# Kernel optimization log

Hardware: AMD Instinct MI355X
Metric: run time of the kernel (lower is better)

## Reference

```python
import jax, jax.numpy as jnp
import numpy as np

KB, KI = 6, 0   # kernel quantizer: quantized_bits(6, 0, alpha=1)
BB, BI = 6, 0   # bias quantizer:   quantized_bits(6, 0, alpha=1)
AB, AI = 6, 0   # activation:       quantized_relu(6, 0)


def _round_ste(p):
    # straight-through round (QKeras _round_through); tf.round and jnp.round
    # both round half-to-even
    return p + jax.lax.stop_gradient(jnp.round(p) - p)


def quantized_bits(x, bits, integer):
    # QKeras quantized_bits with keep_negative=1, symmetric=0, alpha=1
    m = float(2 ** (bits - 1))      # non-sign levels
    m_i = float(2 ** integer)
    p = x * (m / m_i)
    return (m_i / m) * jnp.clip(_round_ste(p), -m, m - 1.0)


def quantized_relu(x, bits, integer):
    # QKeras quantized_relu with negative_slope=0, use_sigmoid=0
    m = float(2 ** bits)
    m_i = float(2 ** integer)
    p = x * (m / m_i)
    return (m_i / m) * jnp.clip(_round_ste(p), 0.0, m - 1.0)


def setup_inputs() -> dict:
    key = jax.random.key(0)
    ks = jax.random.split(key, 9)
    dims = [128, 1024, 2048, 4096, 4096]
    inp = {"x": jax.random.normal(ks[0], (8192, dims[0]), dtype=jnp.float32)}
    for i in range(4):
        fan_in, fan_out = dims[i], dims[i + 1]
        scale = np.sqrt(2.0 / (fan_in + fan_out))  # glorot-ish scale
        inp[f"W{i}"] = jax.random.normal(ks[1 + 2 * i], (fan_in, fan_out), dtype=jnp.float32) * scale
        inp[f"b{i}"] = jax.random.normal(ks[2 + 2 * i], (fan_out,), dtype=jnp.float32) * 0.01
    return inp


def reference(x, W0, b0, W1, b1, W2, b2, W3, b3):
    Ws = [W0, W1, W2, W3]
    bs = [b0, b1, b2, b3]
    h = x
    for i in range(4):
        wq = quantized_bits(Ws[i], KB, KI)
        bq = quantized_bits(bs[i], BB, BI)
        h = jnp.dot(h, wq) + bq
        if i != 3:  # last layer has activation=None
            h = quantized_relu(h, AB, AI)
    return h
```

## Files before the change

kernel.cpp:

```cpp
#include <hip/hip_runtime.h>
#include <stdint.h>

typedef int v4i __attribute__((ext_vector_type(4)));

__device__ __forceinline__ float qlevel(float x) {
  float p = rintf(x * 32.0f);
  return fminf(fmaxf(p, -32.0f), 31.0f);
}

__device__ __forceinline__ int8_t qrelu_level(float p) {
  int q = (int)rintf(p);
  q = q < 0 ? 0 : (q > 63 ? 63 : q);
  return (int8_t)q;
}

__device__ __forceinline__ void async16(const void* g, void* l) {
  __builtin_amdgcn_global_load_lds(
      (const __attribute__((address_space(1))) void*)g,
      (__attribute__((address_space(3))) void*)l, 16, 0, 0);
}

__global__ __launch_bounds__(256) void quant_w0_k(const float* __restrict__ W,
                                                  int8_t* __restrict__ wq) {
  int i = blockIdx.x * 256 + threadIdx.x;
  float4 v = ((const float4*)W)[i];
  char4 c;
  c.x = (int8_t)(int)qlevel(v.x);
  c.y = (int8_t)(int)qlevel(v.y);
  c.z = (int8_t)(int)qlevel(v.z);
  c.w = (int8_t)(int)qlevel(v.w);
  ((char4*)wq)[i] = c;
}

__global__ __launch_bounds__(256) void quantT_k(const float* __restrict__ W,
                                                int8_t* __restrict__ wt,
                                                int K, int N) {
  const int t = threadIdx.x;
  const int l = t & 63;
  const int kc = t >> 6;
  const int k0 = blockIdx.y * 64 + kc * 16;
  const int n = blockIdx.x * 64 + l;
  union { int8_t b[16]; int4 v; } u;
#pragma unroll
  for (int j = 0; j < 16; ++j)
    u.b[j] = (int8_t)(int)qlevel(W[(size_t)(k0 + j) * N + n]);
  *(int4*)&wt[(size_t)n * K + k0] = u.v;
}

__global__ __launch_bounds__(256) void quant_bias_k(
    const float* __restrict__ b0, const float* __restrict__ b1,
    const float* __restrict__ b2, const float* __restrict__ b3,
    float* __restrict__ o0, float* __restrict__ o1,
    float* __restrict__ o2, float* __restrict__ o3) {
  int i = blockIdx.x * 256 + threadIdx.x;
  if (i < 1024) o0[i] = qlevel(b0[i]);
  if (i < 2048) o1[i] = qlevel(b1[i]);
  o2[i] = qlevel(b2[i]);
  o3[i] = qlevel(b3[i]);
}

__global__ __launch_bounds__(256) void layer0_k(const float* __restrict__ x,
                                                const int8_t* __restrict__ w0q,
                                                const float* __restrict__ bint,
                                                int8_t* __restrict__ a1) {
  const int K = 128, N = 1024;
  __shared__ float xs[64][132];
  __shared__ int8_t wsm[128][64];
  const int tid = threadIdx.x;
  const int m0 = blockIdx.y * 64;
  const int n0 = blockIdx.x * 64;
#pragma unroll
  for (int i = 0; i < 8; ++i) {
    int idx = tid + 256 * i;
    int row = idx >> 5, c4 = idx & 31;
    float4 v = *(const float4*)(x + (size_t)(m0 + row) * K + c4 * 4);
    *(float4*)&xs[row][c4 * 4] = v;
  }
#pragma unroll
  for (int i = 0; i < 8; ++i) {
    int idx = tid + 256 * i;
    int k = idx >> 4, c4 = idx & 15;
    *(int*)&wsm[k][c4 * 4] = *(const int*)(w0q + (size_t)k * N + n0 + c4 * 4);
  }
  __syncthreads();
  const int ty = tid >> 4, tx = tid & 15;
  float acc[4][4] = {};
  for (int k4 = 0; k4 < K; k4 += 4) {
    float xr[4][4];
#pragma unroll
    for (int i = 0; i < 4; ++i) {
      float4 v = *(const float4*)&xs[ty * 4 + i][k4];
      xr[i][0] = v.x; xr[i][1] = v.y; xr[i][2] = v.z; xr[i][3] = v.w;
    }
#pragma unroll
    for (int kk = 0; kk < 4; ++kk) {
      char4 cv = *(const char4*)&wsm[k4 + kk][tx * 4];
      float w0 = (float)cv.x, w1 = (float)cv.y, w2 = (float)cv.z, w3 = (float)cv.w;
#pragma unroll
      for (int i = 0; i < 4; ++i) {
        acc[i][0] = fmaf(xr[i][kk], w0, acc[i][0]);
        acc[i][1] = fmaf(xr[i][kk], w1, acc[i][1]);
        acc[i][2] = fmaf(xr[i][kk], w2, acc[i][2]);
        acc[i][3] = fmaf(xr[i][kk], w3, acc[i][3]);
      }
    }
  }
  const int n = n0 + tx * 4;
  float b0v = 2.0f * bint[n + 0], b1v = 2.0f * bint[n + 1];
  float b2v = 2.0f * bint[n + 2], b3v = 2.0f * bint[n + 3];
#pragma unroll
  for (int i = 0; i < 4; ++i) {
    int m = m0 + ty * 4 + i;
    char4 o;
    o.x = qrelu_level(2.0f * acc[i][0] + b0v);
    o.y = qrelu_level(2.0f * acc[i][1] + b1v);
    o.z = qrelu_level(2.0f * acc[i][2] + b2v);
    o.w = qrelu_level(2.0f * acc[i][3] + b3v);
    *(char4*)&a1[(size_t)m * 1024 + n] = o;
  }
}

template <bool FINAL>
__global__ __launch_bounds__(512) void gemm_i8(const int8_t* __restrict__ A,
                                               const int8_t* __restrict__ BT,
                                               const float* __restrict__ bint,
                                               void* __restrict__ outp,
                                               int M, int N, int K) {
  __shared__ __align__(16) int8_t ldsA[3][256 * 64];
  __shared__ __align__(16) int8_t ldsB[3][256 * 64];
  const int tid = threadIdx.x;
  const int wid = tid >> 6;
  const int lane = tid & 63;
  const int wm = wid >> 2, wn = wid & 3;
  const int quad = lane >> 4, r = lane & 15;
  const int m0 = blockIdx.y * 256, n0 = blockIdx.x * 256;

  const int8_t* Ab = A + (size_t)m0 * K;
  const int8_t* Bb = BT + (size_t)n0 * K;

  const int srow = tid >> 2;
  const int sp = tid & 3;
  const int skc = (sp - (srow >> 1)) & 3;
  const int8_t* gA0 = Ab + (size_t)srow * K + skc * 16;
  const int8_t* gA1 = Ab + (size_t)(srow + 128) * K + skc * 16;
  const int8_t* gB0 = Bb + (size_t)srow * K + skc * 16;
  const int8_t* gB1 = Bb + (size_t)(srow + 128) * K + skc * 16;
  const int ldsOff0 = (wid * 64) * 16;
  const int ldsOff1 = (512 + wid * 64) * 16;

  const int pfrag = (quad + (r >> 1)) & 3;

  v4i acc[8][4] = {};

#define STAGE(buf, kt)                                \
  do {                                                \
    async16(gA0 + (kt) * 64, &ldsA[buf][ldsOff0]);    \
    async16(gA1 + (kt) * 64, &ldsA[buf][ldsOff1]);    \
    async16(gB0 + (kt) * 64, &ldsB[buf][ldsOff0]);    \
    async16(gB1 + (kt) * 64, &ldsB[buf][ldsOff1]);    \
  } while (0)

#define ITER(p, q, kt, doStage, vmN)                                          \
  do {                                                                        \
    __builtin_amdgcn_s_barrier();                                             \
    v4i bf[4], af0[4], af1[4];                                                \
    const int8_t* La_ = &ldsA[p][0];                                          \
    const int8_t* Lb_ = &ldsB[p][0];                                          \
    _Pragma("unroll")                                                         \
    for (int nt = 0; nt < 4; ++nt)                                            \
      bf[nt] = *(const v4i*)&Lb_[(wn * 64 + nt * 16 + r) * 64 + pfrag * 16];  \
    _Pragma("unroll")                                                         \
    for (int mt = 0; mt < 4; ++mt)                                            \
      af0[mt] = *(const v4i*)&La_[(wm * 128 + mt * 16 + r) * 64 + pfrag * 16];\
    _Pragma("unroll")                                                         \
    for (int mt = 0; mt < 4; ++mt)                                            \
      af1[mt] = *(const v4i*)&La_[(wm * 128 + 64 + mt * 16 + r) * 64 +        \
                                  pfrag * 16];                                \
    if (doStage) STAGE(q, kt);                                                \
    __builtin_amdgcn_s_setprio(1);                                            \
    _Pragma("unroll")                                                         \
    for (int mt = 0; mt < 4; ++mt)                                            \
      _Pragma("unroll")                                                       \
      for (int nt = 0; nt < 4; ++nt)                                          \
        acc[mt][nt] = __builtin_amdgcn_mfma_i32_16x16x64_i8(                  \
            af0[mt], bf[nt], acc[mt][nt], 0, 0, 0);                           \
    _Pragma("unroll")                                                         \
    for (int mt = 0; mt < 4; ++mt)                                            \
      _Pragma("unroll")                                                       \
      for (int nt = 0; nt < 4; ++nt)                                          \
        acc[4 + mt][nt] = __builtin_amdgcn_mfma_i32_16x16x64_i8(              \
            af1[mt], bf[nt], acc[4 + mt][nt], 0, 0, 0);                       \
    __builtin_amdgcn_s_setprio(0);                                            \
    if (vmN == 4) asm volatile("s_waitcnt vmcnt(4)" ::: "memory");            \
    if (vmN == 0) asm volatile("s_waitcnt vmcnt(0)" ::: "memory");            \
  } while (0)

  const int NT = K >> 6;

  STAGE(0, 0);
  STAGE(1, 1);
  asm volatile("s_waitcnt vmcnt(4)" ::: "memory");

  for (int t = 0; t < NT - 2; ++t) {
    ITER(t % 3, (t + 2) % 3, t + 2, true, 4);
  }
  ITER((NT - 2) % 3, 0, 0, false, 0);
  ITER((NT - 1) % 3, 0, 0, false, -1);

#undef ITER
#undef STAGE

  const int mbase = m0 + wm * 128;
  const int nbase = n0 + wn * 64;
  if (FINAL) {
    float* out = (float*)outp;
#pragma unroll
    for (int nt = 0; nt < 4; ++nt) {
      int n = nbase + nt * 16 + r;
      float bq = bint[n] * 0.03125f;
#pragma unroll
      for (int mt = 0; mt < 8; ++mt)
#pragma unroll
        for (int g = 0; g < 4; ++g) {
          int m = mbase + mt * 16 + quad * 4 + g;
          out[(size_t)m * N + n] = (float)acc[mt][nt][g] * (1.0f / 2048.0f) + bq;
        }
    }
  } else {
    int8_t* out = (int8_t*)outp;
#pragma unroll
    for (int nt = 0; nt < 4; ++nt) {
      int n = nbase + nt * 16 + r;
      float b2 = 2.0f * bint[n];
#pragma unroll
      for (int mt = 0; mt < 8; ++mt)
#pragma unroll
        for (int g = 0; g < 4; ++g) {
          int m = mbase + mt * 16 + quad * 4 + g;
          out[(size_t)m * N + n] =
              qrelu_level((float)acc[mt][nt][g] * 0.03125f + b2);
        }
    }
  }
}

extern "C" void kernel_launch(void* const* d_in, const int* in_sizes, int n_in,
                              void* d_out, int out_size, void* d_ws, size_t ws_size,
                              hipStream_t stream) {
  const float* x  = (const float*)d_in[0];
  const float* W0 = (const float*)d_in[1];
  const float* b0 = (const float*)d_in[2];
  const float* W1 = (const float*)d_in[3];
  const float* b1 = (const float*)d_in[4];
  const float* W2 = (const float*)d_in[5];
  const float* b2 = (const float*)d_in[6];
  const float* W3 = (const float*)d_in[7];
  const float* b3 = (const float*)d_in[8];

  uint8_t* ws = (uint8_t*)d_ws;
  int8_t* wq0 = (int8_t*)(ws + 0);
  int8_t* wt1 = (int8_t*)(ws + 131072);
  int8_t* wt2 = (int8_t*)(ws + 2228224);
  int8_t* wt3 = (int8_t*)(ws + 10616832);
  float*  bq0 = (float*)(ws + 27394048);
  float*  bq1 = (float*)(ws + 27398144);
  float*  bq2 = (float*)(ws + 27406336);
  float*  bq3 = (float*)(ws + 27422720);
  int8_t* a1  = (int8_t*)(ws + 27439104);
  int8_t* a2  = (int8_t*)(ws + 35827712);
  int8_t* a3  = (int8_t*)(ws + 52604928);

  quant_w0_k<<<128, 256, 0, stream>>>(W0, wq0);
  quantT_k<<<dim3(2048 / 64, 1024 / 64), 256, 0, stream>>>(W1, wt1, 1024, 2048);
  quantT_k<<<dim3(4096 / 64, 2048 / 64), 256, 0, stream>>>(W2, wt2, 2048, 4096);
  quantT_k<<<dim3(4096 / 64, 4096 / 64), 256, 0, stream>>>(W3, wt3, 4096, 4096);
  quant_bias_k<<<16, 256, 0, stream>>>(b0, b1, b2, b3, bq0, bq1, bq2, bq3);
  layer0_k<<<dim3(16, 128), 256, 0, stream>>>(x, wq0, bq0, a1);
  gemm_i8<false><<<dim3(2048 / 256, 8192 / 256), 512, 0, stream>>>(
      a1, wt1, bq1, a2, 8192, 2048, 1024);
  gemm_i8<false><<<dim3(4096 / 256, 8192 / 256), 512, 0, stream>>>(
      a2, wt2, bq2, a3, 8192, 4096, 2048);
  gemm_i8<true><<<dim3(4096 / 256, 8192 / 256), 512, 0, stream>>>(
      a3, wt3, bq3, d_out, 8192, 4096, 4096);
}
```

Measured before the change: 459.8 us.

## Software-pipeline LDS fragment reads with MFMA via register double-buffering

The int8 GEMM main loop now keeps the A and B fragments for the current k-tile in a register array. The LDS reads for the next k-tile are interleaved between the MFMA groups, so LDS latency overlaps with matrix math instead of running as a separate read phase before the MFMAs. The global-to-LDS staging is issued at the top of each iteration. Each iteration now ends with a full vmcnt(0) wait and a barrier, which shortens how far the global prefetch can run ahead and adds register pressure from the live fragment array.

```diff
diff --git a/kernel.cpp b/kernel.cpp
--- a/kernel.cpp
+++ b/kernel.cpp
@@ -151,6 +151,7 @@
   const int pfrag = (quad + (r >> 1)) & 3;
 
   v4i acc[8][4] = {};
+  v4i fr[12];
 
 #define STAGE(buf, kt)                                \
   do {                                                \
@@ -160,54 +161,70 @@
     async16(gB1 + (kt) * 64, &ldsB[buf][ldsOff1]);    \
   } while (0)
 
-#define ITER(p, q, kt, doStage, vmN)                                          \
+#define RDA0(Lx, mt) (*(const v4i*)&(Lx)[(wm * 128 + (mt) * 16 + r) * 64 + pfrag * 16])
+#define RDA1(Lx, mt) (*(const v4i*)&(Lx)[(wm * 128 + 64 + (mt) * 16 + r) * 64 + pfrag * 16])
+#define RDB(Lx, nt)  (*(const v4i*)&(Lx)[(wn * 64 + (nt) * 16 + r) * 64 + pfrag * 16])
+
+#define MG(ai, ar)                                                            \
+  _Pragma("unroll")                                                           \
+  for (int nt = 0; nt < 4; ++nt)                                              \
+    acc[ar][nt] = __builtin_amdgcn_mfma_i32_16x16x64_i8(fr[ai], fr[nt],       \
+                                                        acc[ar][nt], 0, 0, 0);
+
+#define BODY(REF, LnA, LnB)                                                   \
   do {                                                                        \
-    __builtin_amdgcn_s_barrier();                                             \
-    v4i bf[4], af0[4], af1[4];                                                \
-    const int8_t* La_ = &ldsA[p][0];                                          \
-    const int8_t* Lb_ = &ldsB[p][0];                                          \
-    _Pragma("unroll")                                                         \
-    for (int nt = 0; nt < 4; ++nt)                                            \
-      bf[nt] = *(const v4i*)&Lb_[(wn * 64 + nt * 16 + r) * 64 + pfrag * 16];  \
-    _Pragma("unroll")                                                         \
-    for (int mt = 0; mt < 4; ++mt)                                            \
-      af0[mt] = *(const v4i*)&La_[(wm * 128 + mt * 16 + r) * 64 + pfrag * 16];\
-    _Pragma("unroll")                                                         \
-    for (int mt = 0; mt < 4; ++mt)                                            \
-      af1[mt] = *(const v4i*)&La_[(wm * 128 + 64 + mt * 16 + r) * 64 +        \
-                                  pfrag * 16];                                \
-    if (doStage) STAGE(q, kt);                                                \
     __builtin_amdgcn_s_setprio(1);                                            \
-    _Pragma("unroll")                                                         \
-    for (int mt = 0; mt < 4; ++mt)                                            \
-      _Pragma("unroll")                                                       \
-      for (int nt = 0; nt < 4; ++nt)                                          \
-        acc[mt][nt] = __builtin_amdgcn_mfma_i32_16x16x64_i8(                  \
-            af0[mt], bf[nt], acc[mt][nt], 0, 0, 0);                           \
-    _Pragma("unroll")                                                         \
-    for (int mt = 0; mt < 4; ++mt)                                            \
-      _Pragma("unroll")                                                       \
-      for (int nt = 0; nt < 4; ++nt)                                          \
-        acc[4 + mt][nt] = __builtin_amdgcn_mfma_i32_16x16x64_i8(              \
-            af1[mt], bf[nt], acc[4 + mt][nt], 0, 0, 0);                       \
+    MG(4, 0);  if (REF) fr[4]  = RDA0(LnA, 0);                                \
+    MG(5, 1);  if (REF) fr[5]  = RDA0(LnA, 1);                                \
+    MG(6, 2);  if (REF) fr[6]  = RDA0(LnA, 2);                                \
+    MG(7, 3);  if (REF) fr[7]  = RDA0(LnA, 3);                                \
+    MG(8, 4);  if (REF) fr[8]  = RDA1(LnA, 0);                                \
+    MG(9, 5);  if (REF) fr[9]  = RDA1(LnA, 1);                                \
+    MG(10, 6); if (REF) fr[10] = RDA1(LnA, 2);                                \
+    MG(11, 7); if (REF) fr[11] = RDA1(LnA, 3);                                \
+    if (REF) {                                                                \
+      fr[0] = RDB(LnB, 0); fr[1] = RDB(LnB, 1);                               \
+      fr[2] = RDB(LnB, 2); fr[3] = RDB(LnB, 3);                               \
+    }                                                                         \
     __builtin_amdgcn_s_setprio(0);                                            \
-    if (vmN == 4) asm volatile("s_waitcnt vmcnt(4)" ::: "memory");            \
-    if (vmN == 0) asm volatile("s_waitcnt vmcnt(0)" ::: "memory");            \
   } while (0)
 
   const int NT = K >> 6;
 
   STAGE(0, 0);
   STAGE(1, 1);
-  asm volatile("s_waitcnt vmcnt(4)" ::: "memory");
-
-  for (int t = 0; t < NT - 2; ++t) {
-    ITER(t % 3, (t + 2) % 3, t + 2, true, 4);
-  }
-  ITER((NT - 2) % 3, 0, 0, false, 0);
-  ITER((NT - 1) % 3, 0, 0, false, -1);
-
-#undef ITER
+  asm volatile("s_waitcnt vmcnt(0)" ::: "memory");
+  __builtin_amdgcn_s_barrier();
+  {
+    const int8_t* L0a = &ldsA[0][0];
+    const int8_t* L0b = &ldsB[0][0];
+    fr[0] = RDB(L0b, 0); fr[1] = RDB(L0b, 1);
+    fr[2] = RDB(L0b, 2); fr[3] = RDB(L0b, 3);
+    fr[4] = RDA0(L0a, 0); fr[5] = RDA0(L0a, 1);
+    fr[6] = RDA0(L0a, 2); fr[7] = RDA0(L0a, 3);
+    fr[8] = RDA1(L0a, 0); fr[9] = RDA1(L0a, 1);
+    fr[10] = RDA1(L0a, 2); fr[11] = RDA1(L0a, 3);
+  }
+
+  for (int t = 0; t < NT - 1; ++t) {
+    if (t + 2 < NT) STAGE((t + 2) % 3, t + 2);
+    const int8_t* LnA = &ldsA[(t + 1) % 3][0];
+    const int8_t* LnB = &ldsB[(t + 1) % 3][0];
+    BODY(true, LnA, LnB);
+    asm volatile("s_waitcnt vmcnt(0)" ::: "memory");
+    __builtin_amdgcn_s_barrier();
+  }
+  {
+    const int8_t* LnA = &ldsA[0][0];
+    const int8_t* LnB = &ldsB[0][0];
+    BODY(false, LnA, LnB);
+  }
+
+#undef BODY
+#undef MG
+#undef RDA0
+#undef RDA1
+#undef RDB
 #undef STAGE
 
   const int mbase = m0 + wm * 128;
```

Measured after the change: 507.4 us. 10.3% more time.
